# Kernel optimization log

Measured on AMD Instinct MI355X. Metric: run time of the kernel, lower is better.

The kernel has to match this reference:

```python
import jax, jax.numpy as jnp
import numpy as np


def setup_inputs() -> dict:
    key = jax.random.key(0)
    k1, k2, k3 = jax.random.split(key, 3)
    B, N, D = 4, 256, 128
    s = jax.random.normal(k1, (B, N, D), dtype=jnp.float32)
    W1 = jax.random.normal(k2, (3 * D, 2 * D), dtype=jnp.float32) * 0.02
    b1 = jnp.zeros((2 * D,), dtype=jnp.float32)
    W2 = jax.random.normal(k3, (2 * D, 1), dtype=jnp.float32) * 0.02
    b2 = jnp.zeros((1,), dtype=jnp.float32)
    return {"s": s, "W1": W1, "b1": b1, "W2": W2, "b2": b2, "K": 8}


def reference(s, W1, b1, W2, b2, K):
    B, N, D = s.shape
    si = jnp.broadcast_to(s[:, :, None, :], (B, N, N, D))
    sj = jnp.broadcast_to(s[:, None, :, :], (B, N, N, D))
    pair = jnp.concatenate([si, sj, si * sj], axis=-1)  # [B,N,N,3D]
    h = jax.nn.relu(pair @ W1 + b1)                      # [B,N,N,2D]
    scores = (h @ W2 + b2)[..., 0]                       # [B,N,N]
    k = min(int(K), N)
    _, idx = jax.lax.top_k(scores, k)                    # [B,N,K]
    # scatter ones at topk indices (indices are distinct per row)
    gate = jnp.sum(jax.nn.one_hot(idx, N, dtype=jnp.float32), axis=-2)  # [B,N,N]
    w = gate / jnp.clip(jnp.sum(gate, axis=-1, keepdims=True), 1.0)
    ctx = jnp.einsum('bij,bjd->bid', w, s)               # [B,N,D]
    return ctx, gate, w
```

## Files before the change

kernel.cpp:

```cpp
#include <hip/hip_runtime.h>
#include <hip/hip_bf16.h>
#include <math.h>

#define B_ 4
#define N_ 256
#define D_ 128
#define H_ 256
#define K_ 8

typedef __attribute__((ext_vector_type(8))) short short8;
typedef __attribute__((ext_vector_type(4))) float f32x4;

__device__ __forceinline__ unsigned short f2bf(float x) {
    union { __hip_bfloat16 h; unsigned short s; } u;
    u.h = __float2bfloat16(x);
    return u.s;
}
__device__ __forceinline__ float bf2f(unsigned short b) {
    unsigned v = ((unsigned)b) << 16;
    return __builtin_bit_cast(float, v);
}
__device__ __forceinline__ unsigned pk2(float x, float y) {
    union { __hip_bfloat162 h; unsigned u; } c;
    c.h = __float22bfloat162_rn(float2{x, y});
    return c.u;
}

__global__ __launch_bounds__(256) void pre_kernel(
    const float* __restrict__ s, const float* __restrict__ W1,
    const float* __restrict__ b1,
    float* __restrict__ avec, float* __restrict__ bvec,
    unsigned short* __restrict__ Wt)
{
    int blk = blockIdx.x;
    int t = threadIdx.x;
    if (blk < 512) {
        int bi0 = blk * 2;
        __shared__ float s2[2][D_];
        {
            int r = t >> 7, d = t & 127;
            s2[r][d] = s[(size_t)(bi0 + r) * D_ + d];
        }
        __syncthreads();
        float aA0 = b1[t], aA1 = aA0, aB0 = 0.f, aB1 = 0.f;
        const float* W1a = W1 + t;
        const float* W1b = W1 + (size_t)D_ * H_ + t;
        #pragma unroll 8
        for (int d = 0; d < D_; ++d) {
            float wa = W1a[(size_t)d * H_];
            float wb = W1b[(size_t)d * H_];
            float s0 = s2[0][d], s1 = s2[1][d];
            aA0 = fmaf(s0, wa, aA0);
            aA1 = fmaf(s1, wa, aA1);
            aB0 = fmaf(s0, wb, aB0);
            aB1 = fmaf(s1, wb, aB1);
        }
        avec[(size_t)bi0 * H_ + t]       = aA0;
        avec[(size_t)(bi0 + 1) * H_ + t] = aA1;
        bvec[(size_t)bi0 * H_ + t]       = aB0;
        bvec[(size_t)(bi0 + 1) * H_ + t] = aB1;
    } else {
        int e = (blk - 512) * 256 + t;
        int h = e >> 7, d = e & 127;
        Wt[e] = f2bf(W1[(size_t)(2 * D_ + d) * H_ + h]);
    }
}

__global__ __launch_bounds__(512, 2) void approx_scores(
    const float* __restrict__ s, const unsigned short* __restrict__ Wt,
    const float* __restrict__ W2, const float* __restrict__ b2,
    const float* __restrict__ avec, const float* __restrict__ bvec,
    unsigned short* __restrict__ ascu)
{
    int blk = blockIdx.x;
    int b   = blk >> 6;
    int jtb = ((blk >> 4) & 3) * 64;
    int i0  = (blk & 15) * 16;
    int t = threadIdx.x;
    int lane = t & 63;
    int w = __builtin_amdgcn_readfirstlane(t >> 6);
    int l15 = lane & 15, quad = lane >> 4;

    __shared__ __align__(16) short Pl[2][64 * 128];
    __shared__ __align__(16) float si_all[16][D_];
    __shared__ float partial[2][8][64];

    const float* sB = s + (size_t)b * N_ * D_;

    {
        int ii = t >> 5, dq = t & 31;
        *(float4*)&si_all[ii][dq * 4] =
            *(const float4*)(sB + (size_t)(i0 + ii) * D_ + dq * 4);
    }

    short8 Wreg[2][4];
    #pragma unroll
    for (int mi = 0; mi < 2; ++mi)
        #pragma unroll
        for (int dk = 0; dk < 4; ++dk)
            Wreg[mi][dk] = *(const short8*)(
                Wt + (size_t)(w * 32 + mi * 16 + l15) * D_ + dk * 32 + quad * 8);
    float bvr[2][4][4];
    float w2r[2][4];
    #pragma unroll
    for (int mi = 0; mi < 2; ++mi) {
        int hq = w * 32 + mi * 16 + quad * 4;
        #pragma unroll
        for (int r = 0; r < 4; ++r)
            w2r[mi][r] = W2[hq + r];
        #pragma unroll
        for (int nj = 0; nj < 4; ++nj)
            #pragma unroll
            for (int r = 0; r < 4; ++r)
                bvr[mi][nj][r] = bvec[((size_t)(b * N_ + jtb + nj * 16 + l15)) * H_
                                      + hq + r];
    }
    float b2v = b2[0];
    __syncthreads();

    {
        int row = t >> 3, seg = t & 7;
        const float* sj = sB + (size_t)(jtb + row) * D_ + seg * 16;
        float4 a0 = ((const float4*)sj)[0], a1 = ((const float4*)sj)[1];
        float4 a2 = ((const float4*)sj)[2], a3 = ((const float4*)sj)[3];
        const float* si = &si_all[0][seg * 16];
        float4 s0 = ((const float4*)si)[0], s1 = ((const float4*)si)[1];
        float4 s2 = ((const float4*)si)[2], s3 = ((const float4*)si)[3];
        uint4 v0, v1;
        v0.x = pk2(a0.x * s0.x, a0.y * s0.y); v0.y = pk2(a0.z * s0.z, a0.w * s0.w);
        v0.z = pk2(a1.x * s1.x, a1.y * s1.y); v0.w = pk2(a1.z * s1.z, a1.w * s1.w);
        v1.x = pk2(a2.x * s2.x, a2.y * s2.y); v1.y = pk2(a2.z * s2.z, a2.w * s2.w);
        v1.z = pk2(a3.x * s3.x, a3.y * s3.y); v1.w = pk2(a3.z * s3.z, a3.w * s3.w);
        int pc0 = (seg * 2) ^ (row & 15), pc1 = (seg * 2 + 1) ^ (row & 15);
        *(uint4*)&Pl[0][row * 128 + pc0 * 8] = v0;
        *(uint4*)&Pl[0][row * 128 + pc1 * 8] = v1;
    }
    __syncthreads();

    #pragma unroll 1
    for (int i = 0; i < 16; ++i) {
        int cur = i & 1;
        if (w == 0 && i > 0) {
            float sum = b2v;
            #pragma unroll
            for (int ww = 0; ww < 8; ++ww) sum += partial[(i - 1) & 1][ww][lane];
            ascu[(size_t)(b * N_ + i0 + i - 1) * N_ + jtb + lane] = f2bf(sum);
        }
        float avc[2][4];
        #pragma unroll
        for (int mi = 0; mi < 2; ++mi) {
            int hq = w * 32 + mi * 16 + quad * 4;
            #pragma unroll
            for (int r = 0; r < 4; ++r)
                avc[mi][r] = avec[(size_t)(b * N_ + i0 + i) * H_ + hq + r];
        }
        f32x4 acc[2][4];
        #pragma unroll
        for (int mi = 0; mi < 2; ++mi)
            #pragma unroll
            for (int nj = 0; nj < 4; ++nj)
                acc[mi][nj] = (f32x4){0.f, 0.f, 0.f, 0.f};
        #pragma unroll
        for (int dk = 0; dk < 4; ++dk) {
            short8 Pf[4];
            #pragma unroll
            for (int nj = 0; nj < 4; ++nj) {
                int pcc = (dk * 4 + quad) ^ l15;
                Pf[nj] = *(const short8*)&Pl[cur][(nj * 16 + l15) * 128 + pcc * 8];
            }
            #pragma unroll
            for (int nj = 0; nj < 4; ++nj)
                #pragma unroll
                for (int mi = 0; mi < 2; ++mi)
                    acc[mi][nj] = __builtin_amdgcn_mfma_f32_16x16x32_bf16(
                        Wreg[mi][dk], Pf[nj], acc[mi][nj], 0, 0, 0);
        }
        if (i < 15) {
            int row = t >> 3, seg = t & 7;
            const float* sj = sB + (size_t)(jtb + row) * D_ + seg * 16;
            float4 a0 = ((const float4*)sj)[0], a1 = ((const float4*)sj)[1];
            float4 a2 = ((const float4*)sj)[2], a3 = ((const float4*)sj)[3];
            const float* si = &si_all[i + 1][seg * 16];
            float4 s0 = ((const float4*)si)[0], s1 = ((const float4*)si)[1];
            float4 s2 = ((const float4*)si)[2], s3 = ((const float4*)si)[3];
            uint4 v0, v1;
            v0.x = pk2(a0.x * s0.x, a0.y * s0.y); v0.y = pk2(a0.z * s0.z, a0.w * s0.w);
            v0.z = pk2(a1.x * s1.x, a1.y * s1.y); v0.w = pk2(a1.z * s1.z, a1.w * s1.w);
            v1.x = pk2(a2.x * s2.x, a2.y * s2.y); v1.y = pk2(a2.z * s2.z, a2.w * s2.w);
            v1.z = pk2(a3.x * s3.x, a3.y * s3.y); v1.w = pk2(a3.z * s3.z, a3.w * s3.w);
            int pc0 = (seg * 2) ^ (row & 15), pc1 = (seg * 2 + 1) ^ (row & 15);
            *(uint4*)&Pl[cur ^ 1][row * 128 + pc0 * 8] = v0;
            *(uint4*)&Pl[cur ^ 1][row * 128 + pc1 * 8] = v1;
        }
        float rs[4];
        #pragma unroll
        for (int nj = 0; nj < 4; ++nj) rs[nj] = 0.f;
        #pragma unroll
        for (int mi = 0; mi < 2; ++mi)
            #pragma unroll
            for (int nj = 0; nj < 4; ++nj)
                #pragma unroll
                for (int r = 0; r < 4; ++r) {
                    float z = acc[mi][nj][r] + avc[mi][r] + bvr[mi][nj][r];
                    rs[nj] = fmaf(fmaxf(z, 0.f), w2r[mi][r], rs[nj]);
                }
        #pragma unroll
        for (int nj = 0; nj < 4; ++nj) {
            rs[nj] += __shfl_xor(rs[nj], 16);
            rs[nj] += __shfl_xor(rs[nj], 32);
        }
        float v = (quad == 0) ? rs[0] : (quad == 1) ? rs[1] : (quad == 2) ? rs[2] : rs[3];
        partial[cur][w][lane] = v;
        __syncthreads();
    }
    if (w == 0) {
        float sum = b2v;
        #pragma unroll
        for (int ww = 0; ww < 8; ++ww) sum += partial[15 & 1][ww][lane];
        ascu[(size_t)(b * N_ + i0 + 15) * N_ + jtb + lane] = f2bf(sum);
    }
}

#define DCH 32
__global__ __launch_bounds__(512, 4) void finalize_kernel(
    const float* __restrict__ s, const float* __restrict__ W1,
    const float* __restrict__ W2, const float* __restrict__ b2,
    const float* __restrict__ avec, const float* __restrict__ bvec,
    const unsigned short* __restrict__ ascu,
    float* __restrict__ ctx, float* __restrict__ gate, float* __restrict__ w)
{
    int bi0 = blockIdx.x * 2;
    int b = bi0 >> 8;
    int t = threadIdx.x;

    __shared__ float asc[2][N_];
    __shared__ int cand[2][16];
    __shared__ __align__(16) float Pt[D_][32];
    __shared__ __align__(16) float Wl[DCH][H_];
    __shared__ float part[32][33];
    __shared__ float rsc[2][16];
    __shared__ int sel8[2][8];

    {
        int tr = t >> 8, jj = t & 255;
        asc[tr][jj] = bf2f(ascu[(size_t)(bi0 + tr) * N_ + jj]);
    }
    __syncthreads();
    {
        int tr = t >> 8, jj = t & 255;
        float my = asc[tr][jj];
        int rank = 0;
        #pragma unroll 8
        for (int j2 = 0; j2 < N_; ++j2) {
            float o = asc[tr][j2];
            rank += (o > my) || (o == my && j2 < jj);
        }
        if (rank < 16) cand[tr][rank] = jj;
    }
    __syncthreads();

    const float* Wc = W1 + (size_t)2 * D_ * H_;

    float4 wpre[4];
    #pragma unroll
    for (int k = 0; k < 4; ++k) {
        int q = t + 512 * k;
        int dd = q >> 6, hh = (q & 63) * 4;
        wpre[k] = *(const float4*)(Wc + (size_t)dd * H_ + hh);
    }

    #pragma unroll
    for (int e = t; e < 1024; e += 512) {
        int p = e & 31, dq = e >> 5;
        int r = p >> 4, c = p & 15;
        int j = cand[r][c];
        float4 sj = *(const float4*)(s + ((size_t)(b * N_ + j)) * D_ + dq * 4);
        float4 si = *(const float4*)(s + ((size_t)(bi0 + r)) * D_ + dq * 4);
        Pt[dq * 4 + 0][p] = si.x * sj.x;
        Pt[dq * 4 + 1][p] = si.y * sj.y;
        Pt[dq * 4 + 2][p] = si.z * sj.z;
        Pt[dq * 4 + 3][p] = si.w * sj.w;
    }

    int pg = t & 15, hg = t >> 4;
    int h0 = hg * 8;
    float acc[2][8];
    #pragma unroll
    for (int pp = 0; pp < 2; ++pp) {
        int p = pg * 2 + pp;
        int r = p >> 4, c = p & 15;
        int j = cand[r][c];
        const float* av = avec + (size_t)(bi0 + r) * H_ + h0;
        const float* bv = bvec + ((size_t)(b * N_ + j)) * H_ + h0;
        #pragma unroll
        for (int m4 = 0; m4 < 2; ++m4) {
            float4 a4 = *(const float4*)(av + m4 * 4);
            float4 b4 = *(const float4*)(bv + m4 * 4);
            acc[pp][m4 * 4 + 0] = a4.x + b4.x;
            acc[pp][m4 * 4 + 1] = a4.y + b4.y;
            acc[pp][m4 * 4 + 2] = a4.z + b4.z;
            acc[pp][m4 * 4 + 3] = a4.w + b4.w;
        }
    }
    __syncthreads();

    for (int ch = 0; ch < 4; ++ch) {
        #pragma unroll
        for (int k = 0; k < 4; ++k) {
            int q = t + 512 * k;
            int dd = q >> 6, hh = (q & 63) * 4;
            *(float4*)&Wl[dd][hh] = wpre[k];
        }
        __syncthreads();
        if (ch < 3) {
            int d0n = (ch + 1) * DCH;
            #pragma unroll
            for (int k = 0; k < 4; ++k) {
                int q = t + 512 * k;
                int dd = q >> 6, hh = (q & 63) * 4;
                wpre[k] = *(const float4*)(Wc + (size_t)(d0n + dd) * H_ + hh);
            }
        }
        int d0 = ch * DCH;
        #pragma unroll
        for (int d = 0; d < DCH; ++d) {
            float2 pv = *(const float2*)&Pt[d0 + d][pg * 2];
            float wv[8];
            *(float4*)&wv[0] = *(const float4*)&Wl[d][h0];
            *(float4*)&wv[4] = *(const float4*)&Wl[d][h0 + 4];
            #pragma unroll
            for (int m = 0; m < 8; ++m) {
                acc[0][m] = fmaf(pv.x, wv[m], acc[0][m]);
                acc[1][m] = fmaf(pv.y, wv[m], acc[1][m]);
            }
        }
        __syncthreads();
    }

    {
        float w2v[8];
        *(float4*)&w2v[0] = *(const float4*)(W2 + h0);
        *(float4*)&w2v[4] = *(const float4*)(W2 + h0 + 4);
        #pragma unroll
        for (int pp = 0; pp < 2; ++pp) {
            float sc = 0.f;
            #pragma unroll
            for (int m = 0; m < 8; ++m)
                sc = fmaf(fmaxf(acc[pp][m], 0.f), w2v[m], sc);
            part[pg * 2 + pp][hg] = sc;
        }
    }
    __syncthreads();
    if (t < 32) {
        float sum = b2[0];
        #pragma unroll
        for (int m = 0; m < 32; ++m) sum += part[t][m];
        rsc[t >> 4][t & 15] = sum;
    }
    __syncthreads();

    if (t < 32) {
        int rr = t >> 4, cc = t & 15;
        float my = rsc[rr][cc]; int myj = cand[rr][cc];
        int rank = 0;
        #pragma unroll
        for (int c2 = 0; c2 < 16; ++c2) {
            float o = rsc[rr][c2]; int oj = cand[rr][c2];
            rank += (o > my) || (o == my && oj < myj);
        }
        if (rank < 8) sel8[rr][rank] = myj;
    }
    __syncthreads();

    {
        int rr = t >> 8, jj = t & 255;
        float gv = 0.f;
        #pragma unroll
        for (int m = 0; m < 8; ++m)
            gv = (jj == sel8[rr][m]) ? 1.f : gv;
        gate[(size_t)(bi0 + rr) * N_ + jj] = gv;
        w[(size_t)(bi0 + rr) * N_ + jj]    = gv * 0.125f;
    }
    if (t < 256) {
        int rr = t >> 7, d = t & 127;
        float a = 0.f;
        #pragma unroll
        for (int m = 0; m < 8; ++m)
            a += s[((size_t)(b * N_ + sel8[rr][m])) * D_ + d];
        ctx[(size_t)(bi0 + rr) * D_ + d] = a * 0.125f;
    }
}

extern "C" void kernel_launch(void* const* d_in, const int* in_sizes, int n_in,
                              void* d_out, int out_size, void* d_ws, size_t ws_size,
                              hipStream_t stream)
{
    const float* s  = (const float*)d_in[0];
    const float* W1 = (const float*)d_in[1];
    const float* b1 = (const float*)d_in[2];
    const float* W2 = (const float*)d_in[3];
    const float* b2 = (const float*)d_in[4];

    float* avec = (float*)d_ws;
    float* bvec = avec + (size_t)B_ * N_ * H_;
    unsigned short* ascu = (unsigned short*)(bvec + (size_t)B_ * N_ * H_);
    unsigned short* Wtu  = ascu + (size_t)B_ * N_ * N_;

    float* ctx  = (float*)d_out;
    float* gate = ctx + (size_t)B_ * N_ * D_;
    float* wout = gate + (size_t)B_ * N_ * N_;

    pre_kernel<<<640, 256, 0, stream>>>(s, W1, b1, avec, bvec, Wtu);
    approx_scores<<<256, 512, 0, stream>>>(s, Wtu, W2, b2, avec, bvec, ascu);
    finalize_kernel<<<B_ * N_ / 2, 512, 0, stream>>>(s, W1, W2, b2, avec, bvec, ascu,
                                                     ctx, gate, wout);
}
```

Baseline: 141.8 us.

## Restructure finalize kernel to one row per block with async double-buffered weight loads

The finalize kernel now handles one query row per 256-thread block instead of two rows per 512-thread block, so it launches twice as many blocks. The W1 slice is streamed straight into LDS with global_load_lds in 16-row chunks, double-buffered so the next chunk loads while the current one is used. Each thread now accumulates 16 hidden units for a single candidate, replacing 8 units for two candidates. The aim is to hide weight-load latency behind the FMAs and raise occupancy. In exchange each block re-reads the whole weight slice for a single row, which doubles total weight traffic, and correctness relies on the async LDS loads being finished at each barrier.

```diff
diff --git a/kernel.cpp b/kernel.cpp
--- a/kernel.cpp
+++ b/kernel.cpp
@@ -24,6 +24,11 @@
     union { __hip_bfloat162 h; unsigned u; } c;
     c.h = __float22bfloat162_rn(float2{x, y});
     return c.u;
+}
+__device__ __forceinline__ void gld_lds16(const float* g, float* l) {
+    __builtin_amdgcn_global_load_lds(
+        (const __attribute__((address_space(1))) void*)g,
+        (__attribute__((address_space(3))) void*)l, 16, 0, 0);
 }
 
 __global__ __launch_bounds__(256) void pre_kernel(
@@ -221,173 +226,153 @@
     }
 }
 
-#define DCH 32
-__global__ __launch_bounds__(512, 4) void finalize_kernel(
+#define DC2 16
+#define PADT 17
+__global__ __launch_bounds__(256) void finalize_kernel(
     const float* __restrict__ s, const float* __restrict__ W1,
     const float* __restrict__ W2, const float* __restrict__ b2,
     const float* __restrict__ avec, const float* __restrict__ bvec,
     const unsigned short* __restrict__ ascu,
     float* __restrict__ ctx, float* __restrict__ gate, float* __restrict__ w)
 {
-    int bi0 = blockIdx.x * 2;
-    int b = bi0 >> 8;
+    int bi = blockIdx.x;
+    int b = bi >> 8;
     int t = threadIdx.x;
 
-    __shared__ float asc[2][N_];
-    __shared__ int cand[2][16];
-    __shared__ __align__(16) float Pt[D_][32];
-    __shared__ __align__(16) float Wl[DCH][H_];
-    __shared__ float part[32][33];
-    __shared__ float rsc[2][16];
-    __shared__ int sel8[2][8];
-
-    {
-        int tr = t >> 8, jj = t & 255;
-        asc[tr][jj] = bf2f(ascu[(size_t)(bi0 + tr) * N_ + jj]);
-    }
-    __syncthreads();
-    {
-        int tr = t >> 8, jj = t & 255;
-        float my = asc[tr][jj];
+    __shared__ float asc[N_];
+    __shared__ int cand[16];
+    __shared__ __align__(16) float Pt[D_][PADT];
+    __shared__ __align__(16) float Wl[2][DC2 * H_];
+    __shared__ float part[16][17];
+    __shared__ float rsc[16];
+    __shared__ int sel8[8];
+
+    asc[t] = bf2f(ascu[(size_t)bi * N_ + t]);
+    __syncthreads();
+    {
+        float my = asc[t];
         int rank = 0;
         #pragma unroll 8
         for (int j2 = 0; j2 < N_; ++j2) {
-            float o = asc[tr][j2];
-            rank += (o > my) || (o == my && j2 < jj);
-        }
-        if (rank < 16) cand[tr][rank] = jj;
+            float o = asc[j2];
+            rank += (o > my) || (o == my && j2 < t);
+        }
+        if (rank < 16) cand[rank] = t;
     }
     __syncthreads();
 
     const float* Wc = W1 + (size_t)2 * D_ * H_;
 
-    float4 wpre[4];
     #pragma unroll
     for (int k = 0; k < 4; ++k) {
-        int q = t + 512 * k;
-        int dd = q >> 6, hh = (q & 63) * 4;
-        wpre[k] = *(const float4*)(Wc + (size_t)dd * H_ + hh);
-    }
-
-    #pragma unroll
-    for (int e = t; e < 1024; e += 512) {
-        int p = e & 31, dq = e >> 5;
-        int r = p >> 4, c = p & 15;
-        int j = cand[r][c];
+        int slot = t + 256 * k;
+        gld_lds16(Wc + slot * 4, &Wl[0][slot * 4]);
+    }
+
+    for (int e = t; e < 512; e += 256) {
+        int c = e & 15, dq = e >> 4;
+        int j = cand[c];
         float4 sj = *(const float4*)(s + ((size_t)(b * N_ + j)) * D_ + dq * 4);
-        float4 si = *(const float4*)(s + ((size_t)(bi0 + r)) * D_ + dq * 4);
-        Pt[dq * 4 + 0][p] = si.x * sj.x;
-        Pt[dq * 4 + 1][p] = si.y * sj.y;
-        Pt[dq * 4 + 2][p] = si.z * sj.z;
-        Pt[dq * 4 + 3][p] = si.w * sj.w;
-    }
-
-    int pg = t & 15, hg = t >> 4;
-    int h0 = hg * 8;
-    float acc[2][8];
-    #pragma unroll
-    for (int pp = 0; pp < 2; ++pp) {
-        int p = pg * 2 + pp;
-        int r = p >> 4, c = p & 15;
-        int j = cand[r][c];
-        const float* av = avec + (size_t)(bi0 + r) * H_ + h0;
-        const float* bv = bvec + ((size_t)(b * N_ + j)) * H_ + h0;
-        #pragma unroll
-        for (int m4 = 0; m4 < 2; ++m4) {
+        float4 si = *(const float4*)(s + (size_t)bi * D_ + dq * 4);
+        Pt[dq * 4 + 0][c] = si.x * sj.x;
+        Pt[dq * 4 + 1][c] = si.y * sj.y;
+        Pt[dq * 4 + 2][c] = si.z * sj.z;
+        Pt[dq * 4 + 3][c] = si.w * sj.w;
+    }
+
+    int c = t & 15, hg = t >> 4;
+    int h0 = hg * 16;
+    int jc = cand[c];
+    float acc[16];
+    {
+        const float* av = avec + (size_t)bi * H_ + h0;
+        const float* bv = bvec + ((size_t)(b * N_ + jc)) * H_ + h0;
+        #pragma unroll
+        for (int m4 = 0; m4 < 4; ++m4) {
             float4 a4 = *(const float4*)(av + m4 * 4);
             float4 b4 = *(const float4*)(bv + m4 * 4);
-            acc[pp][m4 * 4 + 0] = a4.x + b4.x;
-            acc[pp][m4 * 4 + 1] = a4.y + b4.y;
-            acc[pp][m4 * 4 + 2] = a4.z + b4.z;
-            acc[pp][m4 * 4 + 3] = a4.w + b4.w;
-        }
-    }
-    __syncthreads();
-
-    for (int ch = 0; ch < 4; ++ch) {
-        #pragma unroll
-        for (int k = 0; k < 4; ++k) {
-            int q = t + 512 * k;
-            int dd = q >> 6, hh = (q & 63) * 4;
-            *(float4*)&Wl[dd][hh] = wpre[k];
+            acc[m4 * 4 + 0] = a4.x + b4.x;
+            acc[m4 * 4 + 1] = a4.y + b4.y;
+            acc[m4 * 4 + 2] = a4.z + b4.z;
+            acc[m4 * 4 + 3] = a4.w + b4.w;
+        }
+    }
+    __syncthreads();
+
+    #pragma unroll 1
+    for (int ch = 0; ch < 8; ++ch) {
+        int cur = ch & 1;
+        if (ch < 7) {
+            const float* src = Wc + (size_t)(ch + 1) * DC2 * H_;
+            #pragma unroll
+            for (int k = 0; k < 4; ++k) {
+                int slot = t + 256 * k;
+                gld_lds16(src + slot * 4, &Wl[cur ^ 1][slot * 4]);
+            }
+        }
+        int d0 = ch * DC2;
+        #pragma unroll
+        for (int d = 0; d < DC2; ++d) {
+            float pv = Pt[d0 + d][c];
+            float wv[16];
+            *(float4*)&wv[0]  = *(const float4*)&Wl[cur][d * H_ + h0];
+            *(float4*)&wv[4]  = *(const float4*)&Wl[cur][d * H_ + h0 + 4];
+            *(float4*)&wv[8]  = *(const float4*)&Wl[cur][d * H_ + h0 + 8];
+            *(float4*)&wv[12] = *(const float4*)&Wl[cur][d * H_ + h0 + 12];
+            #pragma unroll
+            for (int m = 0; m < 16; ++m)
+                acc[m] = fmaf(pv, wv[m], acc[m]);
         }
         __syncthreads();
-        if (ch < 3) {
-            int d0n = (ch + 1) * DCH;
-            #pragma unroll
-            for (int k = 0; k < 4; ++k) {
-                int q = t + 512 * k;
-                int dd = q >> 6, hh = (q & 63) * 4;
-                wpre[k] = *(const float4*)(Wc + (size_t)(d0n + dd) * H_ + hh);
-            }
-        }
-        int d0 = ch * DCH;
-        #pragma unroll
-        for (int d = 0; d < DCH; ++d) {
-            float2 pv = *(const float2*)&Pt[d0 + d][pg * 2];
-            float wv[8];
-            *(float4*)&wv[0] = *(const float4*)&Wl[d][h0];
-            *(float4*)&wv[4] = *(const float4*)&Wl[d][h0 + 4];
-            #pragma unroll
-            for (int m = 0; m < 8; ++m) {
-                acc[0][m] = fmaf(pv.x, wv[m], acc[0][m]);
-                acc[1][m] = fmaf(pv.y, wv[m], acc[1][m]);
-            }
-        }
-        __syncthreads();
-    }
-
-    {
-        float w2v[8];
-        *(float4*)&w2v[0] = *(const float4*)(W2 + h0);
-        *(float4*)&w2v[4] = *(const float4*)(W2 + h0 + 4);
-        #pragma unroll
-        for (int pp = 0; pp < 2; ++pp) {
-            float sc = 0.f;
-            #pragma unroll
-            for (int m = 0; m < 8; ++m)
-                sc = fmaf(fmaxf(acc[pp][m], 0.f), w2v[m], sc);
-            part[pg * 2 + pp][hg] = sc;
-        }
-    }
-    __syncthreads();
-    if (t < 32) {
+    }
+
+    {
+        float w2v[16];
+        *(float4*)&w2v[0]  = *(const float4*)(W2 + h0);
+        *(float4*)&w2v[4]  = *(const float4*)(W2 + h0 + 4);
+        *(float4*)&w2v[8]  = *(const float4*)(W2 + h0 + 8);
+        *(float4*)&w2v[12] = *(const float4*)(W2 + h0 + 12);
+        float sc = 0.f;
+        #pragma unroll
+        for (int m = 0; m < 16; ++m)
+            sc = fmaf(fmaxf(acc[m], 0.f), w2v[m], sc);
+        part[c][hg] = sc;
+    }
+    __syncthreads();
+    if (t < 16) {
         float sum = b2[0];
         #pragma unroll
-        for (int m = 0; m < 32; ++m) sum += part[t][m];
-        rsc[t >> 4][t & 15] = sum;
-    }
-    __syncthreads();
-
-    if (t < 32) {
-        int rr = t >> 4, cc = t & 15;
-        float my = rsc[rr][cc]; int myj = cand[rr][cc];
+        for (int m = 0; m < 16; ++m) sum += part[t][m];
+        rsc[t] = sum;
+    }
+    __syncthreads();
+
+    if (t < 16) {
+        float my = rsc[t]; int myj = cand[t];
         int rank = 0;
         #pragma unroll
         for (int c2 = 0; c2 < 16; ++c2) {
-            float o = rsc[rr][c2]; int oj = cand[rr][c2];
+            float o = rsc[c2]; int oj = cand[c2];
             rank += (o > my) || (o == my && oj < myj);
         }
-        if (rank < 8) sel8[rr][rank] = myj;
-    }
-    __syncthreads();
-
-    {
-        int rr = t >> 8, jj = t & 255;
+        if (rank < 8) sel8[rank] = myj;
+    }
+    __syncthreads();
+
+    {
         float gv = 0.f;
         #pragma unroll
         for (int m = 0; m < 8; ++m)
-            gv = (jj == sel8[rr][m]) ? 1.f : gv;
-        gate[(size_t)(bi0 + rr) * N_ + jj] = gv;
-        w[(size_t)(bi0 + rr) * N_ + jj]    = gv * 0.125f;
-    }
-    if (t < 256) {
-        int rr = t >> 7, d = t & 127;
+            gv = (t == sel8[m]) ? 1.f : gv;
+        gate[(size_t)bi * N_ + t] = gv;
+        w[(size_t)bi * N_ + t]    = gv * 0.125f;
+    }
+    if (t < 128) {
         float a = 0.f;
         #pragma unroll
         for (int m = 0; m < 8; ++m)
-            a += s[((size_t)(b * N_ + sel8[rr][m])) * D_ + d];
-        ctx[(size_t)(bi0 + rr) * D_ + d] = a * 0.125f;
+            a += s[((size_t)(b * N_ + sel8[m])) * D_ + t];
+        ctx[(size_t)bi * D_ + t] = a * 0.125f;
     }
 }
 
@@ -412,6 +397,6 @@
 
     pre_kernel<<<640, 256, 0, stream>>>(s, W1, b1, avec, bvec, Wtu);
     approx_scores<<<256, 512, 0, stream>>>(s, Wtu, W2, b2, avec, bvec, ascu);
-    finalize_kernel<<<B_ * N_ / 2, 512, 0, stream>>>(s, W1, W2, b2, avec, bvec, ascu,
-                                                     ctx, gate, wout);
-}
+    finalize_kernel<<<B_ * N_, 256, 0, stream>>>(s, W1, W2, b2, avec, bvec, ascu,
+                                                 ctx, gate, wout);
+}
```

Result: no change. 141.7 us (-0.1%).
